# Kernel optimization log

Measured on AMD Instinct MI355X. Metric: run time of the kernel, lower is better.

The kernel has to match this reference:

```python
import jax, jax.numpy as jnp
import numpy as np

BETA_MAX = 0.01
CD_WEIGHT = 1.0
FIDELITY_WEIGHT = 0.5
BETA = BETA_MAX  # fully annealed (step >= beta_warmup)
EPS = 1e-12


def _pairwise_dist(a, b):
    """Euclidean distance matrix. a: [B,N,3], b: [B,M,3] -> [B,N,M]."""
    a2 = jnp.sum(a * a, axis=-1)                      # [B,N]
    b2 = jnp.sum(b * b, axis=-1)                      # [B,M]
    ab = jnp.einsum('bnd,bmd->bnm', a, b)             # [B,N,M]
    sq = a2[:, :, None] + b2[:, None, :] - 2.0 * ab
    return jnp.sqrt(jnp.maximum(sq, EPS))


def chamfer_distance_l1(pred, full):
    d = _pairwise_dist(pred, full)                    # [B,N,M]
    d_pf = jnp.min(d, axis=2)                         # pred -> full, [B,N]
    d_fp = jnp.min(d, axis=1)                         # full -> pred, [B,M]
    return 0.5 * (jnp.mean(d_pf) + jnp.mean(d_fp))


def fidelity_loss(partial, pred):
    # one-directional: every partial point should have a close predicted point
    d = _pairwise_dist(partial, pred)                 # [B,P,N]
    return jnp.mean(jnp.min(d, axis=2))


def kl_divergence(mu, logvar):
    # -0.5 * E_batch[ sum_dim (1 + logvar - mu^2 - exp(logvar)) ]
    kl = -0.5 * jnp.sum(1.0 + logvar - mu * mu - jnp.exp(logvar), axis=1)
    return jnp.mean(kl)


def setup_inputs() -> dict:
    key = jax.random.key(0)
    k1, k2, k3, k4, k5 = jax.random.split(key, 5)
    B, N, P, D = 8, 8192, 2048, 512
    return {
        'pred': jax.random.normal(k1, (B, N, 3), dtype=jnp.float32),
        'full': jax.random.normal(k2, (B, N, 3), dtype=jnp.float32),
        'partial': jax.random.normal(k3, (B, P, 3), dtype=jnp.float32),
        'mu': jax.random.normal(k4, (B, D), dtype=jnp.float32),
        'logvar': jax.random.normal(k5, (B, D), dtype=jnp.float32) * 0.1,
    }


def reference(pred, full, partial, mu, logvar):
    cd = chamfer_distance_l1(pred, full)
    kl = kl_divergence(mu, logvar)
    fidel = fidelity_loss(partial, pred)
    total = CD_WEIGHT * cd + BETA * kl + FIDELITY_WEIGHT * fidel
    return (total, cd, kl, fidel)
```

## Files before the change

kernel.cpp:

```cpp
#include <hip/hip_runtime.h>
#include <math.h>

#define BATCH 8
#define NPTS  8192
#define PPTS  2048
#define DLAT  512

typedef __attribute__((ext_vector_type(8)))  short short8;
typedef __attribute__((ext_vector_type(16))) float floatx16;

#define SEG      (2 * BATCH * NPTS + BATCH * PPTS)
#define DIR_PF   0
#define DIR_FP   (BATCH * NPTS)
#define DIR_FID  (2 * BATCH * NPTS)
#define OFF_SEG  8

#define CHUNK  512
#define XBLK   512

__device__ __forceinline__ unsigned short f2bf(float f) {
    unsigned int u = __float_as_uint(f);
    return (unsigned short)((u + 0x7FFFu + ((u >> 16) & 1u)) >> 16);
}
__device__ __forceinline__ float bf2f(unsigned short s) {
    return __uint_as_float(((unsigned int)s) << 16);
}

__device__ __forceinline__ floatx16 mfma_v(short8 a, short8 b, floatx16 c) {
    floatx16 d;
    asm("v_mfma_f32_32x32x16_bf16 %0, %1, %2, %3"
        : "=v"(d) : "v"(a), "v"(b), "v"(c));
    return d;
}

__device__ __forceinline__ float min16(floatx16 d, float prev) {
    float a0 = fminf(fminf(d[0],  d[1]),  d[2]);
    float a1 = fminf(fminf(d[3],  d[4]),  d[5]);
    float a2 = fminf(fminf(d[6],  d[7]),  d[8]);
    float a3 = fminf(fminf(d[9],  d[10]), d[11]);
    float a4 = fminf(fminf(d[12], d[13]), d[14]);
    float b0 = fminf(fminf(a0, a1), a2);
    float b1 = fminf(fminf(a3, a4), d[15]);
    return fminf(fminf(b0, b1), prev);
}

__device__ __forceinline__ void encodeY(float y0, float y1, float y2,
                                        uint4* r0, uint4* r1) {
    const unsigned short h0 = f2bf(y0), h1 = f2bf(y1), h2 = f2bf(y2);
    const unsigned short l0 = f2bf(y0 - bf2f(h0));
    const unsigned short l1 = f2bf(y1 - bf2f(h1));
    const unsigned short l2 = f2bf(y2 - bf2f(h2));
    const float yn = fmaf(y0, y0, fmaf(y1, y1, y2 * y2));
    const unsigned short nh = f2bf(yn);
    const unsigned short nl = f2bf(yn - bf2f(nh));
    r0->x = (unsigned int)h0 | ((unsigned int)h1 << 16);
    r0->y = (unsigned int)h2 | ((unsigned int)l0 << 16);
    r0->z = (unsigned int)l1 | ((unsigned int)l2 << 16);
    r0->w = (unsigned int)h0 | ((unsigned int)h1 << 16);
    r1->x = (unsigned int)h2 | ((unsigned int)nh << 16);
    r1->y = (unsigned int)nl;
    r1->z = 0u; r1->w = 0u;
}

__device__ __forceinline__ short8 encodeX(float x0, float x1, float x2,
                                          int half) {
    const float m0 = -2.0f * x0, m1 = -2.0f * x1, m2 = -2.0f * x2;
    const unsigned short h0 = f2bf(m0), h1 = f2bf(m1), h2 = f2bf(m2);
    const unsigned short l0 = f2bf(m0 - bf2f(h0));
    const unsigned short l1 = f2bf(m1 - bf2f(h1));
    const unsigned short l2 = f2bf(m2 - bf2f(h2));
    const unsigned short one = 0x3F80u;
    union { unsigned short u[8]; short8 v; } r;
    if (half == 0) {
        r.u[0] = h0; r.u[1] = h1; r.u[2] = h2; r.u[3] = h0;
        r.u[4] = h1; r.u[5] = h2; r.u[6] = l0; r.u[7] = l1;
    } else {
        r.u[0] = l2; r.u[1] = one; r.u[2] = one; r.u[3] = 0;
        r.u[4] = 0;  r.u[5] = 0;   r.u[6] = 0;   r.u[7] = 0;
    }
    return r.v;
}

__global__ __launch_bounds__(256, 4) void minpass_kernel(
        const float* __restrict__ pred,
        const float* __restrict__ full,
        const float* __restrict__ partial,
        float* __restrict__ wsf,
        int ysplit) {
    const int bid = blockIdx.x;
    const int ys  = bid % ysplit;
    const int r   = bid / ysplit;
    const int b   = r / 36;
    const int s   = r % 36;
    const int yhalf = NPTS / ysplit;

    const int t = threadIdx.x;

    if (bid == 0) {
        if (t < 4) wsf[t] = 0.0f;
        if (t == 4) ((unsigned int*)wsf)[4] = 0u;
    }

    const float* xset; const float* yset; int minoff; int xbase;
    if (s < 16)      { xset = pred;    yset = full; xbase = b*NPTS + s*XBLK;
                       minoff = OFF_SEG + ys*SEG + DIR_PF  + b*NPTS + s*XBLK; }
    else if (s < 32) { xset = full;    yset = pred; xbase = b*NPTS + (s-16)*XBLK;
                       minoff = OFF_SEG + ys*SEG + DIR_FP  + b*NPTS + (s-16)*XBLK; }
    else             { xset = partial; yset = pred; xbase = b*PPTS + (s-32)*XBLK;
                       minoff = OFF_SEG + ys*SEG + DIR_FID + b*PPTS + (s-32)*XBLK; }

    const int lane = t & 63;
    const int wid  = t >> 6;
    const int l31  = lane & 31;
    const int half = lane >> 5;

    __shared__ uint4 sY[2][CHUNK];

    const int xw = wid * 128;
    short8 bf0, bf1, bf2, bf3;
    float xn0, xn1, xn2, xn3;
    {
        const float* xp0 = xset + (size_t)(xbase + xw + l31) * 3;
        const float* xp1 = xset + (size_t)(xbase + xw + 32 + l31) * 3;
        const float* xp2 = xset + (size_t)(xbase + xw + 64 + l31) * 3;
        const float* xp3 = xset + (size_t)(xbase + xw + 96 + l31) * 3;
        const float a0 = xp0[0], a1 = xp0[1], a2 = xp0[2];
        const float b0 = xp1[0], b1 = xp1[1], b2 = xp1[2];
        const float c0 = xp2[0], c1 = xp2[1], c2 = xp2[2];
        const float e0 = xp3[0], e1 = xp3[1], e2 = xp3[2];
        bf0 = encodeX(a0, a1, a2, half);
        bf1 = encodeX(b0, b1, b2, half);
        bf2 = encodeX(c0, c1, c2, half);
        bf3 = encodeX(e0, e1, e2, half);
        xn0 = fmaf(a0, a0, fmaf(a1, a1, a2 * a2));
        xn1 = fmaf(b0, b0, fmaf(b1, b1, b2 * b2));
        xn2 = fmaf(c0, c0, fmaf(c1, c1, c2 * c2));
        xn3 = fmaf(e0, e0, fmaf(e1, e1, e2 * e2));
    }

    const floatx16 zc = {0,0,0,0, 0,0,0,0, 0,0,0,0, 0,0,0,0};
    float cmin0 = 3.4e38f, cmin1 = 3.4e38f, cmin2 = 3.4e38f, cmin3 = 3.4e38f;

    const float* yptsBase = yset + (size_t)(b * NPTS + ys * yhalf) * 3;

    for (int c = 0; c < yhalf; c += CHUNK) {
        __syncthreads();
        for (int i = t; i < CHUNK; i += 256) {
            const float* yp = yptsBase + (size_t)(c + i) * 3;
            uint4 r0, r1;
            encodeY(yp[0], yp[1], yp[2], &r0, &r1);
            sY[0][i] = r0; sY[1][i] = r1;
        }
        __syncthreads();

        const uint4* sYh = &sY[half][0];
        short8 af = *(const short8*)&sYh[l31];
#pragma unroll 4
        for (int j = 0; j < CHUNK / 32; ++j) {
            const short8 afn =
                *(const short8*)&sYh[((j + 1) & (CHUNK/32 - 1)) * 32 + l31];
            const floatx16 d0 = mfma_v(af, bf0, zc);
            const floatx16 d1 = mfma_v(af, bf1, zc);
            cmin0 = min16(d0, cmin0);
            const floatx16 d2 = mfma_v(af, bf2, zc);
            cmin1 = min16(d1, cmin1);
            const floatx16 d3 = mfma_v(af, bf3, zc);
            cmin2 = min16(d2, cmin2);
            cmin3 = min16(d3, cmin3);
            af = afn;
        }
    }

    const float m0 = fminf(cmin0, __shfl_xor(cmin0, 32, 64));
    const float m1 = fminf(cmin1, __shfl_xor(cmin1, 32, 64));
    const float m2 = fminf(cmin2, __shfl_xor(cmin2, 32, 64));
    const float m3 = fminf(cmin3, __shfl_xor(cmin3, 32, 64));
    if (lane < 32) {
        wsf[minoff + xw + l31]      = fmaxf(m0 + xn0, 0.0f);
        wsf[minoff + xw + 32 + l31] = fmaxf(m1 + xn1, 0.0f);
        wsf[minoff + xw + 64 + l31] = fmaxf(m2 + xn2, 0.0f);
        wsf[minoff + xw + 96 + l31] = fmaxf(m3 + xn3, 0.0f);
    }
}

__device__ __forceinline__ float waveReduceSum(float v) {
#pragma unroll
    for (int o = 32; o > 0; o >>= 1) v += __shfl_down(v, o, 64);
    return v;
}

__device__ __forceinline__ float blockReduceSum(float v) {
    __shared__ float wsum[4];
    const int lane = threadIdx.x & 63;
    const int wid  = threadIdx.x >> 6;
    v = waveReduceSum(v);
    if (lane == 0) wsum[wid] = v;
    __syncthreads();
    if (wid == 0) {
        v = (lane < ((int)blockDim.x >> 6)) ? wsum[lane] : 0.0f;
        v = waveReduceSum(v);
    }
    return v;
}

#define NRED_BLOCKS 145
__global__ __launch_bounds__(256) void reduce_finalize_kernel(
        float* __restrict__ wsf,
        const float* __restrict__ mu,
        const float* __restrict__ logvar,
        float* __restrict__ out,
        int ysplit) {
    float* acc = wsf;
    unsigned int* cnt = (unsigned int*)wsf + 4;
    const int bid = blockIdx.x;
    const int t   = threadIdx.x;

    float v = 0.0f;
    int accIdx;
    if (bid < 144) {
        int base;
        if (bid < 64)       { accIdx = 0; base = DIR_PF  + bid * 1024;         }
        else if (bid < 128) { accIdx = 1; base = DIR_FP  + (bid - 64) * 1024;  }
        else                { accIdx = 2; base = DIR_FID + (bid - 128) * 1024; }
#pragma unroll
        for (int k = 0; k < 4; ++k) {
            const int i = OFF_SEG + base + k * 256 + t;
            float mval = wsf[i];
            for (int sg = 1; sg < ysplit; ++sg)
                mval = fminf(mval, wsf[sg * SEG + i]);
            v += sqrtf(fmaxf(mval, 1e-12f));
        }
    } else {
        accIdx = 3;
#pragma unroll
        for (int k = 0; k < BATCH * DLAT / 256; ++k) {
            const int i = k * 256 + t;
            const float m = mu[i];
            const float l = logvar[i];
            v += -0.5f * (1.0f + l - m * m - expf(l));
        }
    }

    v = blockReduceSum(v);
    if (t == 0) {
        atomicAdd(&acc[accIdx], v);
        __threadfence();
        const unsigned int done = atomicAdd(cnt, 1u);
        if (done == NRED_BLOCKS - 1) {
            const float s_pf  = atomicAdd(&acc[0], 0.0f);
            const float s_fp  = atomicAdd(&acc[1], 0.0f);
            const float s_fid = atomicAdd(&acc[2], 0.0f);
            const float s_kl  = atomicAdd(&acc[3], 0.0f);
            const float cd  = 0.5f * (s_pf / (float)(BATCH * NPTS) +
                                      s_fp / (float)(BATCH * NPTS));
            const float fid = s_fid / (float)(BATCH * PPTS);
            const float kl  = s_kl / (float)BATCH;
            out[0] = cd + 0.01f * kl + 0.5f * fid;
            out[1] = cd;
            out[2] = kl;
            out[3] = fid;
        }
    }
}

extern "C" void kernel_launch(void* const* d_in, const int* in_sizes, int n_in,
                              void* d_out, int out_size, void* d_ws, size_t ws_size,
                              hipStream_t stream) {
    const float* pred    = (const float*)d_in[0];
    const float* full    = (const float*)d_in[1];
    const float* partial = (const float*)d_in[2];
    const float* mu      = (const float*)d_in[3];
    const float* logvar  = (const float*)d_in[4];
    float* out = (float*)d_out;
    float* wsf = (float*)d_ws;

    int ysplit = 2;
    if (ws_size >= (size_t)(OFF_SEG + 8 * SEG) * 4) ysplit = 8;
    else if (ws_size >= (size_t)(OFF_SEG + 4 * SEG) * 4) ysplit = 4;

    minpass_kernel<<<8 * 36 * ysplit, 256, 0, stream>>>(pred, full, partial, wsf, ysplit);

    reduce_finalize_kernel<<<NRED_BLOCKS, 256, 0, stream>>>(wsf, mu, logvar, out, ysplit);
}
```

Before: 109.1 us.

## Halve X tile per block, use v_min3 reductions, raise occupancy hint

Each block now covers 256 query points instead of 512, with two 32-row MFMA tiles per wave instead of four, so the grid doubles to 72 segments per batch. The min16 reduction now uses the v_min3_f32 instruction through inline asm, and the launch bounds ask for 5 blocks per CU. The smaller tile lowers register pressure and adds parallelism, but halves the reuse of each LDS Y fragment, and the doubled block count means every Y chunk is encoded and staged twice as often.

```diff
diff --git a/kernel.cpp b/kernel.cpp
--- a/kernel.cpp
+++ b/kernel.cpp
@@ -16,7 +16,7 @@
 #define OFF_SEG  8
 
 #define CHUNK  512
-#define XBLK   512
+#define XBLK   256
 
 __device__ __forceinline__ unsigned short f2bf(float f) {
     unsigned int u = __float_as_uint(f);
@@ -33,15 +33,21 @@
     return d;
 }
 
+__device__ __forceinline__ float min3f(float a, float b, float c) {
+    float d;
+    asm("v_min3_f32 %0, %1, %2, %3" : "=v"(d) : "v"(a), "v"(b), "v"(c));
+    return d;
+}
+
 __device__ __forceinline__ float min16(floatx16 d, float prev) {
-    float a0 = fminf(fminf(d[0],  d[1]),  d[2]);
-    float a1 = fminf(fminf(d[3],  d[4]),  d[5]);
-    float a2 = fminf(fminf(d[6],  d[7]),  d[8]);
-    float a3 = fminf(fminf(d[9],  d[10]), d[11]);
-    float a4 = fminf(fminf(d[12], d[13]), d[14]);
-    float b0 = fminf(fminf(a0, a1), a2);
-    float b1 = fminf(fminf(a3, a4), d[15]);
-    return fminf(fminf(b0, b1), prev);
+    const float p0 = min3f(d[0],  d[1],  d[2]);
+    const float p1 = min3f(d[3],  d[4],  d[5]);
+    const float p2 = min3f(d[6],  d[7],  d[8]);
+    const float p3 = min3f(d[9],  d[10], d[11]);
+    const float p4 = min3f(d[12], d[13], d[14]);
+    const float q0 = min3f(p0, p1, p2);
+    const float q1 = min3f(p3, p4, d[15]);
+    return min3f(q0, q1, prev);
 }
 
 __device__ __forceinline__ void encodeY(float y0, float y1, float y2,
@@ -81,7 +87,7 @@
     return r.v;
 }
 
-__global__ __launch_bounds__(256, 4) void minpass_kernel(
+__global__ __launch_bounds__(256, 5) void minpass_kernel(
         const float* __restrict__ pred,
         const float* __restrict__ full,
         const float* __restrict__ partial,
@@ -90,8 +96,8 @@
     const int bid = blockIdx.x;
     const int ys  = bid % ysplit;
     const int r   = bid / ysplit;
-    const int b   = r / 36;
-    const int s   = r % 36;
+    const int b   = r / 72;
+    const int s   = r % 72;
     const int yhalf = NPTS / ysplit;
 
     const int t = threadIdx.x;
@@ -102,12 +108,12 @@
     }
 
     const float* xset; const float* yset; int minoff; int xbase;
-    if (s < 16)      { xset = pred;    yset = full; xbase = b*NPTS + s*XBLK;
+    if (s < 32)      { xset = pred;    yset = full; xbase = b*NPTS + s*XBLK;
                        minoff = OFF_SEG + ys*SEG + DIR_PF  + b*NPTS + s*XBLK; }
-    else if (s < 32) { xset = full;    yset = pred; xbase = b*NPTS + (s-16)*XBLK;
-                       minoff = OFF_SEG + ys*SEG + DIR_FP  + b*NPTS + (s-16)*XBLK; }
-    else             { xset = partial; yset = pred; xbase = b*PPTS + (s-32)*XBLK;
-                       minoff = OFF_SEG + ys*SEG + DIR_FID + b*PPTS + (s-32)*XBLK; }
+    else if (s < 64) { xset = full;    yset = pred; xbase = b*NPTS + (s-32)*XBLK;
+                       minoff = OFF_SEG + ys*SEG + DIR_FP  + b*NPTS + (s-32)*XBLK; }
+    else             { xset = partial; yset = pred; xbase = b*PPTS + (s-64)*XBLK;
+                       minoff = OFF_SEG + ys*SEG + DIR_FID + b*PPTS + (s-64)*XBLK; }
 
     const int lane = t & 63;
     const int wid  = t >> 6;
@@ -116,30 +122,22 @@
 
     __shared__ uint4 sY[2][CHUNK];
 
-    const int xw = wid * 128;
-    short8 bf0, bf1, bf2, bf3;
-    float xn0, xn1, xn2, xn3;
+    const int xw = wid * 64;
+    short8 bf0, bf1;
+    float xn0, xn1;
     {
         const float* xp0 = xset + (size_t)(xbase + xw + l31) * 3;
         const float* xp1 = xset + (size_t)(xbase + xw + 32 + l31) * 3;
-        const float* xp2 = xset + (size_t)(xbase + xw + 64 + l31) * 3;
-        const float* xp3 = xset + (size_t)(xbase + xw + 96 + l31) * 3;
         const float a0 = xp0[0], a1 = xp0[1], a2 = xp0[2];
         const float b0 = xp1[0], b1 = xp1[1], b2 = xp1[2];
-        const float c0 = xp2[0], c1 = xp2[1], c2 = xp2[2];
-        const float e0 = xp3[0], e1 = xp3[1], e2 = xp3[2];
         bf0 = encodeX(a0, a1, a2, half);
         bf1 = encodeX(b0, b1, b2, half);
-        bf2 = encodeX(c0, c1, c2, half);
-        bf3 = encodeX(e0, e1, e2, half);
         xn0 = fmaf(a0, a0, fmaf(a1, a1, a2 * a2));
         xn1 = fmaf(b0, b0, fmaf(b1, b1, b2 * b2));
-        xn2 = fmaf(c0, c0, fmaf(c1, c1, c2 * c2));
-        xn3 = fmaf(e0, e0, fmaf(e1, e1, e2 * e2));
     }
 
     const floatx16 zc = {0,0,0,0, 0,0,0,0, 0,0,0,0, 0,0,0,0};
-    float cmin0 = 3.4e38f, cmin1 = 3.4e38f, cmin2 = 3.4e38f, cmin3 = 3.4e38f;
+    float cmin0 = 3.4e38f, cmin1 = 3.4e38f;
 
     const float* yptsBase = yset + (size_t)(b * NPTS + ys * yhalf) * 3;
 
@@ -162,24 +160,16 @@
             const floatx16 d0 = mfma_v(af, bf0, zc);
             const floatx16 d1 = mfma_v(af, bf1, zc);
             cmin0 = min16(d0, cmin0);
-            const floatx16 d2 = mfma_v(af, bf2, zc);
             cmin1 = min16(d1, cmin1);
-            const floatx16 d3 = mfma_v(af, bf3, zc);
-            cmin2 = min16(d2, cmin2);
-            cmin3 = min16(d3, cmin3);
             af = afn;
         }
     }
 
     const float m0 = fminf(cmin0, __shfl_xor(cmin0, 32, 64));
     const float m1 = fminf(cmin1, __shfl_xor(cmin1, 32, 64));
-    const float m2 = fminf(cmin2, __shfl_xor(cmin2, 32, 64));
-    const float m3 = fminf(cmin3, __shfl_xor(cmin3, 32, 64));
     if (lane < 32) {
         wsf[minoff + xw + l31]      = fmaxf(m0 + xn0, 0.0f);
         wsf[minoff + xw + 32 + l31] = fmaxf(m1 + xn1, 0.0f);
-        wsf[minoff + xw + 64 + l31] = fmaxf(m2 + xn2, 0.0f);
-        wsf[minoff + xw + 96 + l31] = fmaxf(m3 + xn3, 0.0f);
     }
 }
 
@@ -278,7 +268,7 @@
     if (ws_size >= (size_t)(OFF_SEG + 8 * SEG) * 4) ysplit = 8;
     else if (ws_size >= (size_t)(OFF_SEG + 4 * SEG) * 4) ysplit = 4;
 
-    minpass_kernel<<<8 * 36 * ysplit, 256, 0, stream>>>(pred, full, partial, wsf, ysplit);
+    minpass_kernel<<<8 * 72 * ysplit, 256, 0, stream>>>(pred, full, partial, wsf, ysplit);
 
     reduce_finalize_kernel<<<NRED_BLOCKS, 256, 0, stream>>>(wsf, mu, logvar, out, ysplit);
 }
```

After: 114.9 us. 1.05x slower.
